# Kernel tuning notes

Hardware: AMD Instinct MI355X
Metric: run time of the kernel (lower is better)

Reference implementation:

```python
import jax, jax.numpy as jnp
import numpy as np

BN_EPS = 1e-5
NN_EPS = 1e-8


def _three_nn_interp(xyz1, xyz2, points2):
    # xyz1: [B,N,3], xyz2: [B,S,3], points2: [B,S,D]
    # squared pairwise distances [B,N,S]
    d = (jnp.sum(xyz1 ** 2, -1)[:, :, None]
         + jnp.sum(xyz2 ** 2, -1)[:, None, :]
         - 2.0 * jnp.einsum('bnc,bsc->bns', xyz1, xyz2))
    neg_d3, idx = jax.lax.top_k(-d, 3)          # top-3 smallest dists
    d3 = -neg_d3                                # [B,N,3]
    recip = 1.0 / (d3 + NN_EPS)
    weight = recip / jnp.sum(recip, axis=2, keepdims=True)  # [B,N,3]
    gathered = jax.vmap(lambda p, i: p[i])(points2, idx)    # [B,N,3,D]
    return jnp.sum(gathered * weight[..., None], axis=2)    # [B,N,D]


def _conv_bn_relu(x, w, b, gamma, beta):
    # x: [B,C,N]; 1x1 conv == channel GEMM; BN in training mode (batch stats)
    y = jnp.einsum('oc,bcn->bon', w, x) + b[None, :, None]
    mean = jnp.mean(y, axis=(0, 2), keepdims=True)
    var = jnp.mean((y - mean) ** 2, axis=(0, 2), keepdims=True)
    y = (y - mean) * jax.lax.rsqrt(var + BN_EPS)
    y = y * gamma[None, :, None] + beta[None, :, None]
    return jax.nn.relu(y)


def setup_inputs() -> dict:
    key = jax.random.key(0)
    ks = jax.random.split(key, 8)
    B, N, S, D1, D2 = 8, 8192, 2048, 256, 256
    Cin, C0, C1 = D1 + D2, 256, 256
    return {
        'xyz1': jax.random.normal(ks[0], (B, 3, N), jnp.float32),
        'xyz2': jax.random.normal(ks[1], (B, 3, S), jnp.float32),
        'points1': jax.random.normal(ks[2], (B, D1, N), jnp.float32),
        'points2': jax.random.normal(ks[3], (B, D2, S), jnp.float32),
        'w0': jax.random.normal(ks[4], (C0, Cin), jnp.float32) * (1.0 / np.sqrt(Cin)),
        'b0': jnp.zeros((C0,), jnp.float32),
        'gamma0': jnp.ones((C0,), jnp.float32),
        'beta0': jnp.zeros((C0,), jnp.float32),
        'w1': jax.random.normal(ks[5], (C1, C0), jnp.float32) * (1.0 / np.sqrt(C0)),
        'b1': jnp.zeros((C1,), jnp.float32),
        'gamma1': jnp.ones((C1,), jnp.float32),
        'beta1': jnp.zeros((C1,), jnp.float32),
    }


def reference(xyz1, xyz2, points1, points2, w0, b0, gamma0, beta0, w1, b1, gamma1, beta1):
    x1 = jnp.transpose(xyz1, (0, 2, 1))     # [B,N,3]
    x2 = jnp.transpose(xyz2, (0, 2, 1))     # [B,S,3]
    p2 = jnp.transpose(points2, (0, 2, 1))  # [B,S,D2]
    interp = _three_nn_interp(x1, x2, p2)   # [B,N,D2]
    p1 = jnp.transpose(points1, (0, 2, 1))  # [B,N,D1]
    new_points = jnp.transpose(jnp.concatenate([p1, interp], axis=-1), (0, 2, 1))  # [B,Cin,N]
    h = _conv_bn_relu(new_points, w0, b0, gamma0, beta0)
    return _conv_bn_relu(h, w1, b1, gamma1, beta1)
```

## Files before the change

### kernel.cpp

```cpp
#include <hip/hip_runtime.h>
#include <math.h>

#define B 8
#define N 8192
#define S 2048
#define SCH 1024
#define C 256
#define CIN 512
#define CNT (B * N)
#define NSLOT 1024

typedef unsigned long long ull;
typedef __attribute__((ext_vector_type(8))) short bf16x8;
typedef __attribute__((ext_vector_type(4))) float floatx4;
typedef __attribute__((ext_vector_type(8))) unsigned short ushort8v;
typedef __attribute__((ext_vector_type(4))) unsigned short ushort4v;

__device__ inline unsigned short f2bf(float f) {
  unsigned u = __builtin_bit_cast(unsigned, f);
  u += 0x7FFF + ((u >> 16) & 1);
  return (unsigned short)(u >> 16);
}
__device__ inline float bf2f(unsigned short h) {
  unsigned u = ((unsigned)h) << 16;
  return __builtin_bit_cast(float, u);
}

__device__ inline void load_lds16(const void* g, void* l) {
  __builtin_amdgcn_global_load_lds(
      (const __attribute__((address_space(1))) unsigned int*)g,
      (__attribute__((address_space(3))) unsigned int*)l, 16, 0, 0);
}

__device__ inline void ins3u(ull k, ull& k0, ull& k1, ull& k2) {
  if (k < k2) {
    if (k < k1) {
      k2 = k1;
      if (k < k0) { k1 = k0; k0 = k; } else k1 = k;
    } else k2 = k;
  }
}

__device__ inline unsigned sortkey(float f) {
  unsigned u = __float_as_uint(f);
  return u ^ (((unsigned)((int)u >> 31)) | 0x80000000u);
}
__device__ inline float unsortkey(unsigned u) {
  unsigned m = ((int)u < 0) ? 0x80000000u : 0xFFFFFFFFu;
  return __uint_as_float(u ^ m);
}

#define QDECL(q)                                                            \
  float d0_##q = INFINITY, d1_##q = INFINITY, d2_##q = INFINITY;            \
  int i0_##q = 0, i1_##q = 0, i2_##q = 0;                                   \
  float qx_##q, qy_##q, qz_##q, q2_##q;

#define QLOAD(q)                                                            \
  {                                                                         \
    float ox = p1[nq + q], oy = p1[N + nq + q], oz = p1[2 * N + nq + q];    \
    q2_##q = ox * ox + oy * oy + oz * oz;                                   \
    qx_##q = -2.0f * ox; qy_##q = -2.0f * oy; qz_##q = -2.0f * oz;          \
  }

#define QINS(q)                                                             \
  {                                                                         \
    float d = fmaf(qx_##q, pc.x, fmaf(qy_##q, pc.y, fmaf(qz_##q, pc.z, pc.w))); \
    bool lt0 = d < d0_##q, lt1 = d < d1_##q, lt2 = d < d2_##q;              \
    i2_##q = lt2 ? (lt1 ? i1_##q : s) : i2_##q;                             \
    i1_##q = lt1 ? (lt0 ? i0_##q : s) : i1_##q;                             \
    i0_##q = lt0 ? s : i0_##q;                                              \
    d2_##q = __builtin_amdgcn_fmed3f(d, d1_##q, d2_##q);                    \
    d1_##q = __builtin_amdgcn_fmed3f(d, d0_##q, d1_##q);                    \
    d0_##q = fminf(d, d0_##q);                                              \
  }

#define QSTORE(q)                                                           \
  {                                                                         \
    size_t kb = ((size_t)(grp * 2 + q) * 16 + sub) * 3;                     \
    keys[kb] = ((ull)sortkey(d0_##q) << 32) | (unsigned)i0_##q;             \
    keys[kb + 1] = ((ull)sortkey(d1_##q) << 32) | (unsigned)i1_##q;         \
    keys[kb + 2] = ((ull)sortkey(d2_##q) << 32) | (unsigned)i2_##q;         \
  }

__global__ __launch_bounds__(256, 4) void nn3_kernel(const float* __restrict__ xyz1,
                                                     const float* __restrict__ xyz2,
                                                     const unsigned short* __restrict__ p2t,
                                                     unsigned short* __restrict__ Xb) {
  __shared__ float4 sp[SCH];
  __shared__ int sidx[32][3];
  __shared__ float swt[32][3];
  int b = blockIdx.x >> 8;
  int n0 = (blockIdx.x & 255) * 32;
  const float* p2 = xyz2 + (size_t)b * 3 * S;
  int tid = threadIdx.x;
  int sub = tid & 15, grp = tid >> 4;
  const float* p1 = xyz1 + (size_t)b * 3 * N;
  int nq = n0 + grp * 2;
  QDECL(0) QDECL(1)
  QLOAD(0) QLOAD(1)

  for (int ch = 0; ch < 2; ++ch) {
    if (ch) __syncthreads();
    for (int i = tid; i < SCH; i += 256) {
      int g = ch * SCH + i;
      float px = p2[g], py = p2[S + g], pz = p2[2 * S + g];
      sp[i] = make_float4(px, py, pz, px * px + py * py + pz * pz);
    }
    __syncthreads();
    int sbase = ch * SCH;
    const float4* spp = sp + sub;
    float4 pcA = spp[0];
    float4 pcB = spp[16];
    for (int t = 0; t < SCH / 16 - 2; t += 2) {
      float4 pnA = spp[(t + 2) * 16];
      float4 pnB = spp[(t + 3) * 16];
      {
        float4 pc = pcA;
        int s = sbase + t * 16 + sub;
        QINS(0) QINS(1)
      }
      {
        float4 pc = pcB;
        int s = sbase + (t + 1) * 16 + sub;
        QINS(0) QINS(1)
      }
      pcA = pnA;
      pcB = pnB;
    }
    {
      float4 pc = pcA;
      int s = sbase + (SCH / 16 - 2) * 16 + sub;
      QINS(0) QINS(1)
    }
    {
      float4 pc = pcB;
      int s = sbase + (SCH / 16 - 1) * 16 + sub;
      QINS(0) QINS(1)
    }
  }

  __syncthreads();
  ull* keys = (ull*)sp;
  QSTORE(0) QSTORE(1)
  __syncthreads();
  if (sub < 4) {
#pragma unroll
    for (int q = 0; q < 2; ++q) {
      size_t qb = (size_t)(grp * 2 + q) * 48;
      ull m0 = ~0ull, m1 = ~0ull, m2 = ~0ull;
#pragma unroll
      for (int jj = 0; jj < 4; ++jj) {
        size_t o2 = qb + (size_t)(sub + 4 * jj) * 3;
        ins3u(keys[o2], m0, m1, m2);
        ins3u(keys[o2 + 1], m0, m1, m2);
        ins3u(keys[o2 + 2], m0, m1, m2);
      }
#pragma unroll
      for (int mm = 1; mm <= 2; mm <<= 1) {
        ull e0 = (ull)__shfl_xor((long long)m0, mm);
        ull e1 = (ull)__shfl_xor((long long)m1, mm);
        ull e2 = (ull)__shfl_xor((long long)m2, mm);
        ins3u(e0, m0, m1, m2);
        ins3u(e1, m0, m1, m2);
        ins3u(e2, m0, m1, m2);
      }
      if (sub == 0) {
        float q2v = q ? q2_1 : q2_0;
        int qi = grp * 2 + q;
        float e0 = fmaxf(unsortkey((unsigned)(m0 >> 32)) + q2v, 0.0f);
        float e1 = fmaxf(unsortkey((unsigned)(m1 >> 32)) + q2v, 0.0f);
        float e2 = fmaxf(unsortkey((unsigned)(m2 >> 32)) + q2v, 0.0f);
        float r0 = 1.0f / (e0 + 1e-8f);
        float r1 = 1.0f / (e1 + 1e-8f);
        float r2 = 1.0f / (e2 + 1e-8f);
        float rs = 1.0f / (r0 + r1 + r2);
        sidx[qi][0] = (int)(unsigned)m0;
        sidx[qi][1] = (int)(unsigned)m1;
        sidx[qi][2] = (int)(unsigned)m2;
        swt[qi][0] = r0 * rs;
        swt[qi][1] = r1 * rs;
        swt[qi][2] = r2 * rs;
      }
    }
  }
  __syncthreads();

  int qi = tid >> 3, cc = tid & 7;
  int j0 = sidx[qi][0], j1 = sidx[qi][1], j2 = sidx[qi][2];
  float w0v = swt[qi][0], w1v = swt[qi][1], w2v = swt[qi][2];
  const unsigned short* pb = p2t + (size_t)b * S * 256;
  const unsigned short* r0p = pb + (size_t)j0 * 256;
  const unsigned short* r1p = pb + (size_t)j1 * 256;
  const unsigned short* r2p = pb + (size_t)j2 * 256;
  unsigned short* xp = Xb + ((size_t)b * N + n0 + qi) * 512 + 256;
#pragma unroll
  for (int h = 0; h < 4; ++h) {
    int co = (cc + h * 8) * 8;
    ushort8v v0 = *(const ushort8v*)(r0p + co);
    ushort8v v1 = *(const ushort8v*)(r1p + co);
    ushort8v v2 = *(const ushort8v*)(r2p + co);
    ushort8v o;
#pragma unroll
    for (int i = 0; i < 8; ++i)
      o[i] = f2bf(w0v * bf2f(v0[i]) + w1v * bf2f(v1[i]) + w2v * bf2f(v2[i]));
    *(ushort8v*)(xp + co) = o;
  }
}

__device__ inline void tconv_body(const float* __restrict__ src,
                                  unsigned short* __restrict__ dst,
                                  int cols, int drow, int bx, int by, int bz,
                                  float (*t)[65]) {
  int n0 = bx * 64, c0 = by * 64, b = bz;
  int tid = threadIdx.x, r = tid >> 2, q = tid & 3;
  const float* sp = src + ((size_t)b * 256 + c0 + r) * cols + n0 + q * 16;
#pragma unroll
  for (int i = 0; i < 4; ++i) {
    float4 v = *(const float4*)(sp + i * 4);
    t[r][q * 16 + i * 4 + 0] = v.x;
    t[r][q * 16 + i * 4 + 1] = v.y;
    t[r][q * 16 + i * 4 + 2] = v.z;
    t[r][q * 16 + i * 4 + 3] = v.w;
  }
  __syncthreads();
  unsigned short* dp = dst + ((size_t)b * cols + n0 + r) * drow + c0 + q * 16;
  ushort8v o0, o1;
#pragma unroll
  for (int i = 0; i < 8; ++i) o0[i] = f2bf(t[q * 16 + i][r]);
#pragma unroll
  for (int i = 0; i < 8; ++i) o1[i] = f2bf(t[q * 16 + 8 + i][r]);
  *(ushort8v*)dp = o0;
  *(ushort8v*)(dp + 8) = o1;
}

__global__ __launch_bounds__(256) void prep_kernel(const float* __restrict__ points1,
                                                   const float* __restrict__ points2,
                                                   const float* __restrict__ w0,
                                                   const float* __restrict__ w1,
                                                   unsigned short* __restrict__ Xb,
                                                   unsigned short* __restrict__ p2t,
                                                   unsigned short* __restrict__ w0b,
                                                   unsigned short* __restrict__ w1b) {
  __shared__ float t[64][65];
  int id = blockIdx.x;
  if (id < 4096) {
    tconv_body(points1, Xb, N, 512, id & 127, (id >> 7) & 3, id >> 9, t);
  } else if (id < 5120) {
    id -= 4096;
    tconv_body(points2, p2t, S, 256, id & 31, (id >> 5) & 3, id >> 7, t);
  } else {
    int i = (id - 5120) * 256 + threadIdx.x;
    if (i < C * CIN) w0b[i] = f2bf(w0[i]);
    else {
      int j = i - C * CIN;
      if (j < C * C) w1b[j] = f2bf(w1[j]);
    }
  }
}

__global__ __launch_bounds__(256) void gemm_kernel(const unsigned short* __restrict__ X,
                                                   const unsigned short* __restrict__ Wb,
                                                   const float* __restrict__ bias,
                                                   unsigned short* __restrict__ Y,
                                                   float* __restrict__ psum,
                                                   float* __restrict__ psumsq,
                                                   int Cin) {
  __shared__ unsigned short As[128 * 64];
  __shared__ unsigned short Bs[128 * 64];
  int n0 = blockIdx.x * 128, o0 = blockIdx.y * 128, b = blockIdx.z;
  int tid = threadIdx.x, lane = tid & 63, wid = tid >> 6;
  int wm = wid >> 1, wn = wid & 1;
  floatx4 acc[4][4];
#pragma unroll
  for (int m = 0; m < 4; ++m)
#pragma unroll
    for (int nt = 0; nt < 4; ++nt) acc[m][nt] = (floatx4)(0.0f);

  size_t rsA = (size_t)Cin * 2;
  int chunkSwz = ((lane & 7) ^ ((lane >> 3) & 7)) * 16;
  const char* Abase = (const char*)Wb + (size_t)(o0 + wid * 32 + (lane >> 3)) * rsA + chunkSwz;
  const char* Bbase = (const char*)X + ((size_t)b * N + n0 + wid * 32 + (lane >> 3)) * rsA + chunkSwz;
  size_t rstep8 = 8 * rsA;
  int fr = lane & 15;
  int cbase = lane >> 4;
  int rswz = lane & 7;

  for (int k0 = 0; k0 < Cin; k0 += 64) {
#pragma unroll
    for (int l = 0; l < 4; ++l) {
      load_lds16(Abase + (size_t)k0 * 2 + (size_t)l * rstep8, &As[(wid * 32 + l * 8) * 64]);
      load_lds16(Bbase + (size_t)k0 * 2 + (size_t)l * rstep8, &Bs[(wid * 32 + l * 8) * 64]);
    }
    __syncthreads();
#pragma unroll
    for (int kk = 0; kk < 2; ++kk) {
      int chunk = (cbase + kk * 4) ^ rswz;
      bf16x8 af[4], bfv[4];
#pragma unroll
      for (int m = 0; m < 4; ++m)
        af[m] = *(const bf16x8*)&As[(wm * 64 + m * 16 + fr) * 64 + chunk * 8];
#pragma unroll
      for (int nt = 0; nt < 4; ++nt)
        bfv[nt] = *(const bf16x8*)&Bs[(wn * 64 + nt * 16 + fr) * 64 + chunk * 8];
#pragma unroll
      for (int m = 0; m < 4; ++m)
#pragma unroll
        for (int nt = 0; nt < 4; ++nt)
          acc[m][nt] = __builtin_amdgcn_mfma_f32_16x16x32_bf16(af[m], bfv[nt], acc[m][nt], 0, 0, 0);
    }
    __syncthreads();
  }

  int col = lane & 15, rowq = lane >> 4;
  int slot = ((b * 64 + blockIdx.x) * 2) + wn;
#pragma unroll
  for (int m = 0; m < 4; ++m) {
    int ob = o0 + wm * 64 + m * 16 + rowq * 4;
    float4 bs = *(const float4*)&bias[ob];
    float sj[4] = {0.f, 0.f, 0.f, 0.f}, qj[4] = {0.f, 0.f, 0.f, 0.f};
#pragma unroll
    for (int nt = 0; nt < 4; ++nt) {
      int n = n0 + wn * 64 + nt * 16 + col;
      float y0 = acc[m][nt][0] + bs.x;
      float y1 = acc[m][nt][1] + bs.y;
      float y2 = acc[m][nt][2] + bs.z;
      float y3 = acc[m][nt][3] + bs.w;
      ushort4v v;
      v[0] = f2bf(y0); v[1] = f2bf(y1); v[2] = f2bf(y2); v[3] = f2bf(y3);
      *(ushort4v*)&Y[((size_t)b * N + n) * 256 + ob] = v;
      sj[0] += y0; qj[0] = fmaf(y0, y0, qj[0]);
      sj[1] += y1; qj[1] = fmaf(y1, y1, qj[1]);
      sj[2] += y2; qj[2] = fmaf(y2, y2, qj[2]);
      sj[3] += y3; qj[3] = fmaf(y3, y3, qj[3]);
    }
#pragma unroll
    for (int j = 0; j < 4; ++j) {
#pragma unroll
      for (int d = 1; d <= 8; d <<= 1) {
        sj[j] += __shfl_xor(sj[j], d);
        qj[j] += __shfl_xor(qj[j], d);
      }
    }
    if (col == 0) {
      int c0 = blockIdx.y * 128 + wm * 64 + m * 16 + rowq * 4;
#pragma unroll
      for (int j = 0; j < 4; ++j) {
        psum[(size_t)(c0 + j) * NSLOT + slot] = sj[j];
        psumsq[(size_t)(c0 + j) * NSLOT + slot] = qj[j];
      }
    }
  }
}

__global__ __launch_bounds__(256) void bnparam_kernel(const float* __restrict__ psum,
                                                      const float* __restrict__ psumsq,
                                                      const float* __restrict__ gamma,
                                                      const float* __restrict__ beta,
                                                      float* __restrict__ scale,
                                                      float* __restrict__ shift) {
  int c = blockIdx.x, tid = threadIdx.x;
  const float* ps = psum + (size_t)c * NSLOT;
  const float* pq = psumsq + (size_t)c * NSLOT;
  float s = 0.f, q = 0.f;
#pragma unroll
  for (int i = 0; i < NSLOT / 256; ++i) {
    s += ps[tid + i * 256];
    q += pq[tid + i * 256];
  }
#pragma unroll
  for (int d = 1; d <= 32; d <<= 1) {
    s += __shfl_xor(s, d);
    q += __shfl_xor(q, d);
  }
  __shared__ float ls[4], lq[4];
  int wid = tid >> 6;
  if ((tid & 63) == 0) { ls[wid] = s; lq[wid] = q; }
  __syncthreads();
  if (tid == 0) {
    s = ls[0] + ls[1] + ls[2] + ls[3];
    q = lq[0] + lq[1] + lq[2] + lq[3];
    float m = s * (1.0f / CNT);
    float v = q * (1.0f / CNT) - m * m;
    float sc = gamma[c] * rsqrtf(v + 1e-5f);
    scale[c] = sc;
    shift[c] = beta[c] - m * sc;
  }
}

__global__ __launch_bounds__(256) void bnrelu_kernel(const unsigned short* __restrict__ Y,
                                                     const float* __restrict__ scale,
                                                     const float* __restrict__ shift,
                                                     unsigned short* __restrict__ H) {
  size_t total = (size_t)B * N * 256 / 8;
  for (size_t i = (size_t)blockIdx.x * 256 + threadIdx.x; i < total;
       i += (size_t)gridDim.x * 256) {
    int ob = ((int)i & 31) * 8;
    float4 s0 = *(const float4*)&scale[ob];
    float4 s1 = *(const float4*)&scale[ob + 4];
    float4 h0 = *(const float4*)&shift[ob];
    float4 h1 = *(const float4*)&shift[ob + 4];
    ushort8v v = *(const ushort8v*)&Y[i * 8];
    ushort8v o;
    o[0] = f2bf(fmaxf(fmaf(bf2f(v[0]), s0.x, h0.x), 0.f));
    o[1] = f2bf(fmaxf(fmaf(bf2f(v[1]), s0.y, h0.y), 0.f));
    o[2] = f2bf(fmaxf(fmaf(bf2f(v[2]), s0.z, h0.z), 0.f));
    o[3] = f2bf(fmaxf(fmaf(bf2f(v[3]), s0.w, h0.w), 0.f));
    o[4] = f2bf(fmaxf(fmaf(bf2f(v[4]), s1.x, h1.x), 0.f));
    o[5] = f2bf(fmaxf(fmaf(bf2f(v[5]), s1.y, h1.y), 0.f));
    o[6] = f2bf(fmaxf(fmaf(bf2f(v[6]), s1.z, h1.z), 0.f));
    o[7] = f2bf(fmaxf(fmaf(bf2f(v[7]), s1.w, h1.w), 0.f));
    *(ushort8v*)&H[i * 8] = o;
  }
}

__global__ __launch_bounds__(256) void bnreluT_kernel(const unsigned short* __restrict__ Y,
                                                      const float* __restrict__ scale,
                                                      const float* __restrict__ shift,
                                                      float* __restrict__ out) {
  __shared__ float t[64][65];
  int n0 = blockIdx.x * 64, o0 = blockIdx.y * 64, b = blockIdx.z;
  int tid = threadIdx.x, r = tid >> 2, q = tid & 3;
  const unsigned short* yp = Y + ((size_t)b * N + n0 + r) * 256 + o0 + q * 16;
#pragma unroll
  for (int h = 0; h < 2; ++h) {
    ushort8v v = *(const ushort8v*)(yp + h * 8);
#pragma unroll
    for (int i = 0; i < 8; ++i) {
      int oc = q * 16 + h * 8 + i;
      float f = fmaxf(fmaf(bf2f(v[i]), scale[o0 + oc], shift[o0 + oc]), 0.f);
      t[oc][r] = f;
    }
  }
  __syncthreads();
  float* op = out + ((size_t)b * 256 + o0 + r) * N + n0 + q * 16;
#pragma unroll
  for (int i = 0; i < 4; ++i) {
    float4 v = make_float4(t[r][q * 16 + i * 4 + 0], t[r][q * 16 + i * 4 + 1],
                           t[r][q * 16 + i * 4 + 2], t[r][q * 16 + i * 4 + 3]);
    *(float4*)(op + i * 4) = v;
  }
}

extern "C" void kernel_launch(void* const* d_in, const int* in_sizes, int n_in,
                              void* d_out, int out_size, void* d_ws, size_t ws_size,
                              hipStream_t stream) {
  const float* xyz1 = (const float*)d_in[0];
  const float* xyz2 = (const float*)d_in[1];
  const float* points1 = (const float*)d_in[2];
  const float* points2 = (const float*)d_in[3];
  const float* w0 = (const float*)d_in[4];
  const float* b0 = (const float*)d_in[5];
  const float* g0 = (const float*)d_in[6];
  const float* be0 = (const float*)d_in[7];
  const float* w1 = (const float*)d_in[8];
  const float* b1 = (const float*)d_in[9];
  const float* g1 = (const float*)d_in[10];
  const float* be1 = (const float*)d_in[11];
  float* out = (float*)d_out;

  char* ws = (char*)d_ws;
  float* scale0 = (float*)ws;          ws += 256 * 4;
  float* shift0 = (float*)ws;          ws += 256 * 4;
  float* scale1 = (float*)ws;          ws += 256 * 4;
  float* shift1 = (float*)ws;          ws += 256 * 4;
  float* psum = (float*)ws;            ws += (size_t)C * NSLOT * 4;
  float* psumsq = (float*)ws;          ws += (size_t)C * NSLOT * 4;
  unsigned short* w0b = (unsigned short*)ws;  ws += (size_t)C * CIN * 2;
  unsigned short* w1b = (unsigned short*)ws;  ws += (size_t)C * C * 2;
  unsigned short* p2t = (unsigned short*)ws;  ws += (size_t)B * S * 256 * 2;
  unsigned short* Xb = (unsigned short*)ws;   ws += (size_t)B * N * 512 * 2;
  unsigned short* Yb = (unsigned short*)ws;   ws += (size_t)B * N * 256 * 2;
  unsigned short* Hb = Xb;

  prep_kernel<<<dim3(4096 + 1024 + 768), 256, 0, stream>>>(points1, points2, w0, w1,
                                                           Xb, p2t, w0b, w1b);
  nn3_kernel<<<dim3(B * N / 32), 256, 0, stream>>>(xyz1, xyz2, p2t, Xb);
  gemm_kernel<<<dim3(N / 128, 2, B), 256, 0, stream>>>(Xb, w0b, b0, Yb, psum, psumsq, CIN);
  bnparam_kernel<<<dim3(C), 256, 0, stream>>>(psum, psumsq, g0, be0, scale0, shift0);
  bnrelu_kernel<<<dim3(2048), 256, 0, stream>>>(Yb, scale0, shift0, Hb);
  gemm_kernel<<<dim3(N / 128, 2, B), 256, 0, stream>>>(Hb, w1b, b1, Yb, psum, psumsq, C);
  bnparam_kernel<<<dim3(C), 256, 0, stream>>>(psum, psumsq, g1, be1, scale1, shift1);
  bnreluT_kernel<<<dim3(N / 64, 4, B), 256, 0, stream>>>(Yb, scale1, shift1, out);
}
```

Measured before the change: 208.2 us.

## Split 3-NN search into distance-only pass and threshold candidate-collection pass

The nearest-neighbour kernel now runs a first pass that tracks only the three smallest distances per query with med3/min, no index bookkeeping, and reduces them to a per-query third-smallest threshold. A second pass recomputes the distances and atomically appends every point at or under the threshold into a small shared-memory candidate list. A final sort of that list yields the indices. This removes the per-point index selects from the hot loop, but adds a second sweep over the points, LDS atomics, and a fixed cap of 8 candidates per query that could drop neighbours when distances tie.

```diff
diff --git a/kernel.cpp b/kernel.cpp
--- a/kernel.cpp
+++ b/kernel.cpp
@@ -41,6 +41,14 @@
   }
 }
 
+__device__ inline void insf(float k, float& m0, float& m1, float& m2) {
+  float n1 = __builtin_amdgcn_fmed3f(k, m0, m1);
+  float n2 = __builtin_amdgcn_fmed3f(k, m1, m2);
+  m0 = fminf(k, m0);
+  m1 = n1;
+  m2 = n2;
+}
+
 __device__ inline unsigned sortkey(float f) {
   unsigned u = __float_as_uint(f);
   return u ^ (((unsigned)((int)u >> 31)) | 0x80000000u);
@@ -52,7 +60,6 @@
 
 #define QDECL(q)                                                            \
   float d0_##q = INFINITY, d1_##q = INFINITY, d2_##q = INFINITY;            \
-  int i0_##q = 0, i1_##q = 0, i2_##q = 0;                                   \
   float qx_##q, qy_##q, qz_##q, q2_##q;
 
 #define QLOAD(q)                                                            \
@@ -62,24 +69,14 @@
     qx_##q = -2.0f * ox; qy_##q = -2.0f * oy; qz_##q = -2.0f * oz;          \
   }
 
-#define QINS(q)                                                             \
+#define QINSD(q)                                                            \
   {                                                                         \
     float d = fmaf(qx_##q, pc.x, fmaf(qy_##q, pc.y, fmaf(qz_##q, pc.z, pc.w))); \
-    bool lt0 = d < d0_##q, lt1 = d < d1_##q, lt2 = d < d2_##q;              \
-    i2_##q = lt2 ? (lt1 ? i1_##q : s) : i2_##q;                             \
-    i1_##q = lt1 ? (lt0 ? i0_##q : s) : i1_##q;                             \
-    i0_##q = lt0 ? s : i0_##q;                                              \
-    d2_##q = __builtin_amdgcn_fmed3f(d, d1_##q, d2_##q);                    \
-    d1_##q = __builtin_amdgcn_fmed3f(d, d0_##q, d1_##q);                    \
+    float n1 = __builtin_amdgcn_fmed3f(d, d0_##q, d1_##q);                  \
+    float n2 = __builtin_amdgcn_fmed3f(d, d1_##q, d2_##q);                  \
     d0_##q = fminf(d, d0_##q);                                              \
-  }
-
-#define QSTORE(q)                                                           \
-  {                                                                         \
-    size_t kb = ((size_t)(grp * 2 + q) * 16 + sub) * 3;                     \
-    keys[kb] = ((ull)sortkey(d0_##q) << 32) | (unsigned)i0_##q;             \
-    keys[kb + 1] = ((ull)sortkey(d1_##q) << 32) | (unsigned)i1_##q;         \
-    keys[kb + 2] = ((ull)sortkey(d2_##q) << 32) | (unsigned)i2_##q;         \
+    d1_##q = n1;                                                            \
+    d2_##q = n2;                                                            \
   }
 
 __global__ __launch_bounds__(256, 4) void nn3_kernel(const float* __restrict__ xyz1,
@@ -87,6 +84,10 @@
                                                      const unsigned short* __restrict__ p2t,
                                                      unsigned short* __restrict__ Xb) {
   __shared__ float4 sp[SCH];
+  __shared__ float t2q[32];
+  __shared__ int ccnt[32];
+  __shared__ float cand_d[32][8];
+  __shared__ int cand_s[32][8];
   __shared__ int sidx[32][3];
   __shared__ float swt[32][3];
   int b = blockIdx.x >> 8;
@@ -107,80 +108,107 @@
       sp[i] = make_float4(px, py, pz, px * px + py * py + pz * pz);
     }
     __syncthreads();
-    int sbase = ch * SCH;
     const float4* spp = sp + sub;
-    float4 pcA = spp[0];
-    float4 pcB = spp[16];
-    for (int t = 0; t < SCH / 16 - 2; t += 2) {
-      float4 pnA = spp[(t + 2) * 16];
-      float4 pnB = spp[(t + 3) * 16];
+    float4 pc = spp[0];
+    for (int t = 0; t < SCH / 16 - 1; ++t) {
+      float4 pn = spp[(t + 1) * 16];
+      QINSD(0) QINSD(1)
+      pc = pn;
+    }
+    QINSD(0) QINSD(1)
+  }
+
+  __syncthreads();
+  float* tm = (float*)sp;
+  tm[((grp * 2 + 0) * 16 + sub) * 3 + 0] = d0_0;
+  tm[((grp * 2 + 0) * 16 + sub) * 3 + 1] = d1_0;
+  tm[((grp * 2 + 0) * 16 + sub) * 3 + 2] = d2_0;
+  tm[((grp * 2 + 1) * 16 + sub) * 3 + 0] = d0_1;
+  tm[((grp * 2 + 1) * 16 + sub) * 3 + 1] = d1_1;
+  tm[((grp * 2 + 1) * 16 + sub) * 3 + 2] = d2_1;
+  if (tid < 32) ccnt[tid] = 0;
+  __syncthreads();
+  if (sub < 4) {
+#pragma unroll
+    for (int q = 0; q < 2; ++q) {
+      int qi = grp * 2 + q;
+      float m0 = INFINITY, m1 = INFINITY, m2 = INFINITY;
+#pragma unroll
+      for (int jj = 0; jj < 4; ++jj) {
+        int ss = sub + 4 * jj;
+        insf(tm[(qi * 16 + ss) * 3 + 0], m0, m1, m2);
+        insf(tm[(qi * 16 + ss) * 3 + 1], m0, m1, m2);
+        insf(tm[(qi * 16 + ss) * 3 + 2], m0, m1, m2);
+      }
+#pragma unroll
+      for (int mm = 1; mm <= 2; mm <<= 1) {
+        float e0 = __shfl_xor(m0, mm);
+        float e1 = __shfl_xor(m1, mm);
+        float e2 = __shfl_xor(m2, mm);
+        insf(e0, m0, m1, m2);
+        insf(e1, m0, m1, m2);
+        insf(e2, m0, m1, m2);
+      }
+      if (sub == 0) t2q[qi] = m2;
+    }
+  }
+  __syncthreads();
+  float t2_0 = t2q[grp * 2], t2_1 = t2q[grp * 2 + 1];
+
+  for (int ch = 0; ch < 2; ++ch) {
+    if (ch) __syncthreads();
+    for (int i = tid; i < SCH; i += 256) {
+      int g = ch * SCH + i;
+      float px = p2[g], py = p2[S + g], pz = p2[2 * S + g];
+      sp[i] = make_float4(px, py, pz, px * px + py * py + pz * pz);
+    }
+    __syncthreads();
+    const float4* spp = sp + sub;
+    for (int t = 0; t < SCH / 16; ++t) {
+      float4 pc = spp[t * 16];
+      int s = ch * SCH + t * 16 + sub;
       {
-        float4 pc = pcA;
-        int s = sbase + t * 16 + sub;
-        QINS(0) QINS(1)
+        float d = fmaf(qx_0, pc.x, fmaf(qy_0, pc.y, fmaf(qz_0, pc.z, pc.w)));
+        if (d <= t2_0) {
+          int sl = atomicAdd(&ccnt[grp * 2], 1);
+          if (sl < 8) { cand_d[grp * 2][sl] = d; cand_s[grp * 2][sl] = s; }
+        }
       }
       {
-        float4 pc = pcB;
-        int s = sbase + (t + 1) * 16 + sub;
-        QINS(0) QINS(1)
-      }
-      pcA = pnA;
-      pcB = pnB;
-    }
-    {
-      float4 pc = pcA;
-      int s = sbase + (SCH / 16 - 2) * 16 + sub;
-      QINS(0) QINS(1)
-    }
-    {
-      float4 pc = pcB;
-      int s = sbase + (SCH / 16 - 1) * 16 + sub;
-      QINS(0) QINS(1)
-    }
-  }
-
-  __syncthreads();
-  ull* keys = (ull*)sp;
-  QSTORE(0) QSTORE(1)
-  __syncthreads();
-  if (sub < 4) {
+        float d = fmaf(qx_1, pc.x, fmaf(qy_1, pc.y, fmaf(qz_1, pc.z, pc.w)));
+        if (d <= t2_1) {
+          int sl = atomicAdd(&ccnt[grp * 2 + 1], 1);
+          if (sl < 8) { cand_d[grp * 2 + 1][sl] = d; cand_s[grp * 2 + 1][sl] = s; }
+        }
+      }
+    }
+  }
+  __syncthreads();
+
+  if (sub == 0) {
 #pragma unroll
     for (int q = 0; q < 2; ++q) {
-      size_t qb = (size_t)(grp * 2 + q) * 48;
-      ull m0 = ~0ull, m1 = ~0ull, m2 = ~0ull;
-#pragma unroll
-      for (int jj = 0; jj < 4; ++jj) {
-        size_t o2 = qb + (size_t)(sub + 4 * jj) * 3;
-        ins3u(keys[o2], m0, m1, m2);
-        ins3u(keys[o2 + 1], m0, m1, m2);
-        ins3u(keys[o2 + 2], m0, m1, m2);
-      }
-#pragma unroll
-      for (int mm = 1; mm <= 2; mm <<= 1) {
-        ull e0 = (ull)__shfl_xor((long long)m0, mm);
-        ull e1 = (ull)__shfl_xor((long long)m1, mm);
-        ull e2 = (ull)__shfl_xor((long long)m2, mm);
-        ins3u(e0, m0, m1, m2);
-        ins3u(e1, m0, m1, m2);
-        ins3u(e2, m0, m1, m2);
-      }
-      if (sub == 0) {
-        float q2v = q ? q2_1 : q2_0;
-        int qi = grp * 2 + q;
-        float e0 = fmaxf(unsortkey((unsigned)(m0 >> 32)) + q2v, 0.0f);
-        float e1 = fmaxf(unsortkey((unsigned)(m1 >> 32)) + q2v, 0.0f);
-        float e2 = fmaxf(unsortkey((unsigned)(m2 >> 32)) + q2v, 0.0f);
-        float r0 = 1.0f / (e0 + 1e-8f);
-        float r1 = 1.0f / (e1 + 1e-8f);
-        float r2 = 1.0f / (e2 + 1e-8f);
-        float rs = 1.0f / (r0 + r1 + r2);
-        sidx[qi][0] = (int)(unsigned)m0;
-        sidx[qi][1] = (int)(unsigned)m1;
-        sidx[qi][2] = (int)(unsigned)m2;
-        swt[qi][0] = r0 * rs;
-        swt[qi][1] = r1 * rs;
-        swt[qi][2] = r2 * rs;
-      }
+      int qi = grp * 2 + q;
+      int n = min(ccnt[qi], 8);
+      ull k0 = ~0ull, k1 = ~0ull, k2 = ~0ull;
+      for (int i = 0; i < n; ++i) {
+        ull k = ((ull)sortkey(cand_d[qi][i]) << 32) | (unsigned)cand_s[qi][i];
+        ins3u(k, k0, k1, k2);
+      }
+      float q2v = q ? q2_1 : q2_0;
+      float e0 = fmaxf(unsortkey((unsigned)(k0 >> 32)) + q2v, 0.0f);
+      float e1 = fmaxf(unsortkey((unsigned)(k1 >> 32)) + q2v, 0.0f);
+      float e2 = fmaxf(unsortkey((unsigned)(k2 >> 32)) + q2v, 0.0f);
+      float r0 = 1.0f / (e0 + 1e-8f);
+      float r1 = 1.0f / (e1 + 1e-8f);
+      float r2 = 1.0f / (e2 + 1e-8f);
+      float rs = 1.0f / (r0 + r1 + r2);
+      sidx[qi][0] = (int)(unsigned)k0;
+      sidx[qi][1] = (int)(unsigned)k1;
+      sidx[qi][2] = (int)(unsigned)k2;
+      swt[qi][0] = r0 * rs;
+      swt[qi][1] = r1 * rs;
+      swt[qi][2] = r2 * rs;
     }
   }
   __syncthreads();
```

Measured after the change: 193.6 us. -7.0%, faster.
